# Optimization experiments

Measured on AMD Instinct MI355X. Metric: run time of the kernel, lower is better.

Reference implementation:

```python
import jax, jax.numpy as jnp
import numpy as np

D_MODEL = 1024
N_HEAD = 16
HEAD_DIM = D_MODEL // N_HEAD
ROPE_BASE = 10000.0


def _weight_quant(w):
    # BitNet b1.58 ternary weight quant with per-tensor absmean scale (STE).
    scale = jnp.clip(jnp.mean(jnp.abs(w)), 1e-5, None)
    wq = jnp.clip(jnp.round(w / scale), -1.0, 1.0) * scale
    return w + jax.lax.stop_gradient(wq - w)


def _act_quant(x):
    # Per-token int8 absmax activation quant (STE).
    scale = 127.0 / jnp.clip(jnp.max(jnp.abs(x), axis=-1, keepdims=True), 1e-5, None)
    xq = jnp.clip(jnp.round(x * scale), -128.0, 127.0) / scale
    return x + jax.lax.stop_gradient(xq - x)


def _bitlinear(x, w):
    # y = act_quant(x) @ weight_quant(w).T   (torch Linear convention, no bias)
    return _act_quant(x) @ _weight_quant(w).T


def _rope(x, pos):
    # x: [B, H, T, D]; half-split rotation.
    d = x.shape[-1]
    inv_freq = 1.0 / (ROPE_BASE ** (jnp.arange(0, d, 2, dtype=jnp.float32) / d))
    ang = pos[:, None].astype(jnp.float32) * inv_freq[None, :]  # [T, D/2]
    cos, sin = jnp.cos(ang), jnp.sin(ang)
    x1, x2 = x[..., : d // 2], x[..., d // 2 :]
    return jnp.concatenate([x1 * cos - x2 * sin, x1 * sin + x2 * cos], axis=-1)


def setup_inputs() -> dict:
    key = jax.random.key(0)
    k0, k1, k2, k3, k4 = jax.random.split(key, 5)
    B, T = 2, 2048
    s = 1.0 / np.sqrt(D_MODEL)
    return {
        "x": jax.random.normal(k0, (B, T, D_MODEL), dtype=jnp.float32),
        "Wq": jax.random.normal(k1, (D_MODEL, D_MODEL), dtype=jnp.float32) * s,
        "Wk": jax.random.normal(k2, (D_MODEL, D_MODEL), dtype=jnp.float32) * s,
        "Wv": jax.random.normal(k3, (D_MODEL, D_MODEL), dtype=jnp.float32) * s,
        "Wo": jax.random.normal(k4, (D_MODEL, D_MODEL), dtype=jnp.float32) * s,
    }


def reference(x, Wq, Wk, Wv, Wo):
    B, T, C = x.shape
    pos = jnp.arange(T)
    def heads(y):
        return y.reshape(B, T, N_HEAD, HEAD_DIM).transpose(0, 2, 1, 3)  # [B,H,T,D]
    q = _rope(heads(_bitlinear(x, Wq)), pos)
    k = _rope(heads(_bitlinear(x, Wk)), pos)
    v = heads(_bitlinear(x, Wv))
    scores = jnp.einsum("bhqd,bhkd->bhqk", q, k) / jnp.sqrt(jnp.float32(HEAD_DIM))
    causal = jnp.tril(jnp.ones((T, T), dtype=bool))
    scores = jnp.where(causal[None, None], scores, jnp.finfo(scores.dtype).min)
    att = jax.nn.softmax(scores, axis=-1)
    y = jnp.einsum("bhqk,bhkd->bhqd", att, v)  # [B,H,T,D]
    y = y.transpose(0, 2, 1, 3).reshape(B, T, C)
    return _bitlinear(y, Wo)
```

## Files before the change

kernel.cpp:

```cpp
#include <hip/hip_runtime.h>
#include <hip/hip_bf16.h>
#include <math.h>

typedef __bf16 bf16_t;
typedef signed char i8_t;
typedef __attribute__((ext_vector_type(8))) __bf16 bf16x8;
typedef __attribute__((ext_vector_type(4))) __bf16 bf16x4;
typedef __attribute__((ext_vector_type(4))) float f32x4;
typedef __attribute__((ext_vector_type(4))) int i32x4;

typedef __attribute__((address_space(3))) void lds_void_t;
typedef const __attribute__((address_space(1))) void glb_void_t;
#define GLOAD_LDS(g, l) __builtin_amdgcn_global_load_lds((glb_void_t*)(g), (lds_void_t*)(l), 16, 0, 0)

#define MFMA16(a,b,c) __builtin_amdgcn_mfma_f32_16x16x32_bf16(a,b,c,0,0,0)
#define MFMAI8(a,b,c) __builtin_amdgcn_mfma_i32_16x16x64_i8(a,b,c,0,0,0)

#if __has_builtin(__builtin_amdgcn_exp2f)
#define EXP2F(x) __builtin_amdgcn_exp2f(x)
#else
#define EXP2F(x) exp2f(x)
#endif

static constexpr int TSEQ = 2048;
static constexpr int CDIM = 1024;
#define NEG_BIG (-1.0e30f)
#define Q_PRESCALE 0.18033688011112042f
#define ROPE_C 0.41524101190971284f

__global__ __launch_bounds__(256) void wreduce(const float* __restrict__ W0, const float* __restrict__ W1,
                                               const float* __restrict__ W2, const float* __restrict__ W3,
                                               double* __restrict__ partial) {
  int w = blockIdx.x >> 6, b = blockIdx.x & 63;
  const float* W = (w==0)?W0:(w==1)?W1:(w==2)?W2:W3;
  const float* base = W + (size_t)b * 16384;
  double s = 0.0;
  for (int i = threadIdx.x * 4; i < 16384; i += 1024) {
    float4 v = *(const float4*)(base + i);
    s += (double)fabsf(v.x) + (double)fabsf(v.y) + (double)fabsf(v.z) + (double)fabsf(v.w);
  }
  #pragma unroll
  for (int off = 1; off < 64; off <<= 1) s += __shfl_xor(s, off);
  __shared__ double red[4];
  if ((threadIdx.x & 63) == 0) red[threadIdx.x >> 6] = s;
  __syncthreads();
  if (threadIdx.x == 0) partial[blockIdx.x] = red[0] + red[1] + red[2] + red[3];
}

__global__ __launch_bounds__(256) void prep(const float* __restrict__ W0, const float* __restrict__ W1,
                                            const float* __restrict__ W2, const float* __restrict__ W3,
                                            const double* __restrict__ partial, float* __restrict__ wscale,
                                            i8_t* __restrict__ wq_all,
                                            const float* __restrict__ xg, i8_t* __restrict__ xqg,
                                            float* __restrict__ rowfac, float2* __restrict__ ropetab) {
  int bid = blockIdx.x;
  if (bid < 4096) {
    int w = bid >> 10;
    double ssum = 0.0;
    for (int i = 0; i < 64; ++i) ssum += partial[w * 64 + i];
    float s = fmaxf((float)(ssum * (1.0 / 1048576.0)), 1e-5f);
    if ((bid & 1023) == 0 && threadIdx.x == 0) wscale[w] = s;
    const float* W = (w==0)?W0:(w==1)?W1:(w==2)?W2:W3;
    int off = ((bid & 1023) * 256 + threadIdx.x) * 4;
    float4 v = *(const float4*)(W + off);
    char4 q;
    q.x = (i8_t)(int)fminf(fmaxf(rintf(v.x / s), -1.f), 1.f);
    q.y = (i8_t)(int)fminf(fmaxf(rintf(v.y / s), -1.f), 1.f);
    q.z = (i8_t)(int)fminf(fmaxf(rintf(v.z / s), -1.f), 1.f);
    q.w = (i8_t)(int)fminf(fmaxf(rintf(v.w / s), -1.f), 1.f);
    *(char4*)(wq_all + (size_t)w * 1048576 + off) = q;
  } else if (bid < 8192) {
    int r = bid - 4096;
    float4 v = *(const float4*)(xg + (size_t)r * 1024 + threadIdx.x * 4);
    float mx = fmaxf(fmaxf(fabsf(v.x), fabsf(v.y)), fmaxf(fabsf(v.z), fabsf(v.w)));
    #pragma unroll
    for (int off = 1; off < 64; off <<= 1) mx = fmaxf(mx, __shfl_xor(mx, off));
    __shared__ float red[4];
    if ((threadIdx.x & 63) == 0) red[threadIdx.x >> 6] = mx;
    __syncthreads();
    mx = fmaxf(fmaxf(red[0], red[1]), fmaxf(red[2], red[3]));
    mx = fmaxf(mx, 1e-5f);
    float scale = 127.0f / mx;
    if (threadIdx.x == 0) rowfac[r] = mx * (1.0f / 127.0f);
    char4 q;
    q.x = (i8_t)(int)fminf(fmaxf(rintf(v.x * scale), -128.f), 127.f);
    q.y = (i8_t)(int)fminf(fmaxf(rintf(v.y * scale), -128.f), 127.f);
    q.z = (i8_t)(int)fminf(fmaxf(rintf(v.z * scale), -128.f), 127.f);
    q.w = (i8_t)(int)fminf(fmaxf(rintf(v.w * scale), -128.f), 127.f);
    *(char4*)(xqg + (size_t)r * 1024 + threadIdx.x * 4) = q;
  } else {
    int t = (bid - 8192) * 8 + (threadIdx.x >> 5);
    int ii = threadIdx.x & 31;
    float ang = (float)t * exp2f(-(float)ii * ROPE_C);
    float sn, cs;
    sincosf(ang, &sn, &cs);
    ropetab[t * 32 + ii] = make_float2(cs, sn);
  }
}

__global__ __launch_bounds__(256) void actquant(const float* __restrict__ xg, i8_t* __restrict__ xqg,
                                                float* __restrict__ rowfac) {
  int r = blockIdx.x;
  float4 v = *(const float4*)(xg + (size_t)r * 1024 + threadIdx.x * 4);
  float mx = fmaxf(fmaxf(fabsf(v.x), fabsf(v.y)), fmaxf(fabsf(v.z), fabsf(v.w)));
  #pragma unroll
  for (int off = 1; off < 64; off <<= 1) mx = fmaxf(mx, __shfl_xor(mx, off));
  __shared__ float red[4];
  if ((threadIdx.x & 63) == 0) red[threadIdx.x >> 6] = mx;
  __syncthreads();
  mx = fmaxf(fmaxf(red[0], red[1]), fmaxf(red[2], red[3]));
  mx = fmaxf(mx, 1e-5f);
  float scale = 127.0f / mx;
  if (threadIdx.x == 0) rowfac[r] = mx * (1.0f / 127.0f);
  char4 q;
  q.x = (i8_t)(int)fminf(fmaxf(rintf(v.x * scale), -128.f), 127.f);
  q.y = (i8_t)(int)fminf(fmaxf(rintf(v.y * scale), -128.f), 127.f);
  q.z = (i8_t)(int)fminf(fmaxf(rintf(v.z * scale), -128.f), 127.f);
  q.w = (i8_t)(int)fminf(fmaxf(rintf(v.w * scale), -128.f), 127.f);
  *(char4*)(xqg + (size_t)r * 1024 + threadIdx.x * 4) = q;
}

__global__ __launch_bounds__(256) void gemm_qkv(const i8_t* __restrict__ xq, const i8_t* __restrict__ wq_all,
                                                const float* __restrict__ wscale, const float* __restrict__ rowfac,
                                                const float2* __restrict__ ropetab,
                                                bf16_t* __restrict__ qb, bf16_t* __restrict__ kb,
                                                bf16_t* __restrict__ vtb) {
  const int z = blockIdx.z;
  const i8_t* Bw = wq_all + (size_t)z * 1048576;
  const int m0 = blockIdx.x * 128, n0 = blockIdx.y * 128;
  const int tid = threadIdx.x;
  const int wave = tid >> 6, lane = tid & 63, quad = lane >> 4, l16 = lane & 15;
  const int wm = wave >> 1, wn = wave & 1;
  __shared__ __align__(16) i8_t As[2][128 * 64];
  __shared__ __align__(16) i8_t Bs[2][128 * 64];
  i32x4 zero = {0, 0, 0, 0};
  i32x4 acc[4][4];
  #pragma unroll
  for (int i = 0; i < 4; ++i)
    #pragma unroll
    for (int j = 0; j < 4; ++j) acc[i][j] = zero;

  const int row_s = tid >> 2;
  const int cg16 = (((tid & 3) - (row_s >> 1)) & 3) * 16;
  const int sw16 = ((quad + (l16 >> 1)) & 3) * 16;

  #pragma unroll
  for (int v2 = 0; v2 < 2; ++v2) {
    int v = tid + v2 * 256;
    int row = row_s + v2 * 64;
    GLOAD_LDS(&xq[(size_t)(m0 + row) * 1024 + cg16], &As[0][v * 16]);
    GLOAD_LDS(&Bw[(size_t)(n0 + row) * 1024 + cg16], &Bs[0][v * 16]);
  }
  __syncthreads();

  #pragma unroll 2
  for (int kt = 0; kt < 16; ++kt) {
    const int cur = kt & 1;
    if (kt < 15) {
      #pragma unroll
      for (int v2 = 0; v2 < 2; ++v2) {
        int v = tid + v2 * 256;
        int row = row_s + v2 * 64;
        GLOAD_LDS(&xq[(size_t)(m0 + row) * 1024 + (kt + 1) * 64 + cg16], &As[cur ^ 1][v * 16]);
        GLOAD_LDS(&Bw[(size_t)(n0 + row) * 1024 + (kt + 1) * 64 + cg16], &Bs[cur ^ 1][v * 16]);
      }
    }
    i32x4 af[4], bfr[4];
    #pragma unroll
    for (int i = 0; i < 4; ++i) af[i] = *(const i32x4*)&As[cur][(wm * 64 + i * 16 + l16) * 64 + sw16];
    #pragma unroll
    for (int j = 0; j < 4; ++j) bfr[j] = *(const i32x4*)&Bs[cur][(wn * 64 + j * 16 + l16) * 64 + sw16];
    if (z == 2) {
      #pragma unroll
      for (int i = 0; i < 4; ++i)
        #pragma unroll
        for (int j = 0; j < 4; ++j) acc[i][j] = MFMAI8(bfr[i], af[j], acc[i][j]);
    } else {
      #pragma unroll
      for (int i = 0; i < 4; ++i)
        #pragma unroll
        for (int j = 0; j < 4; ++j) acc[i][j] = MFMAI8(af[i], bfr[j], acc[i][j]);
    }
    __syncthreads();
  }
  float ws = wscale[z] * (z == 0 ? Q_PRESCALE : 1.0f);
  if (z <= 1) {
    bf16_t* dst = (z == 0) ? qb : kb;
    const int h = (n0 >> 6) + wn;
    #pragma unroll
    for (int i = 0; i < 4; ++i) {
      #pragma unroll
      for (int r = 0; r < 4; ++r) {
        int m = m0 + wm * 64 + i * 16 + quad * 4 + r;
        float rf = rowfac[m] * ws;
        int b = m >> 11, t = m & 2047;
        bf16_t* drow = dst + (((size_t)b * 16 + h) * 2048 + t) * 64;
        #pragma unroll
        for (int j = 0; j < 2; ++j) {
          int dd1 = j * 16 + l16;
          float2 cs2 = ropetab[t * 32 + dd1];
          float v1 = (float)acc[i][j][r] * rf;
          float v2 = (float)acc[i][j + 2][r] * rf;
          drow[dd1]      = (bf16_t)(v1 * cs2.x - v2 * cs2.y);
          drow[dd1 + 32] = (bf16_t)(v1 * cs2.y + v2 * cs2.x);
        }
      }
    }
  } else {
    const int b = m0 >> 11;
    const int tbase = (m0 & 2047) + wm * 64;
    float rfj[4];
    #pragma unroll
    for (int j = 0; j < 4; ++j) rfj[j] = rowfac[m0 + wm * 64 + j * 16 + l16] * ws;
    #pragma unroll
    for (int i = 0; i < 4; ++i) {
      #pragma unroll
      for (int r = 0; r < 4; ++r) {
        int nrow = n0 + wn * 64 + i * 16 + quad * 4 + r;
        int h = nrow >> 6, dd = nrow & 63;
        bf16_t* vrow = vtb + (((size_t)b * 16 + h) * 64 + dd) * 2048 + tbase;
        #pragma unroll
        for (int j = 0; j < 4; ++j) vrow[j * 16 + l16] = (bf16_t)((float)acc[i][j][r] * rfj[j]);
      }
    }
  }
}

__global__ __launch_bounds__(256) void gemm_out(const i8_t* __restrict__ yq, const i8_t* __restrict__ wo,
                                                const float* __restrict__ wscale, const float* __restrict__ rowfac,
                                                float* __restrict__ out) {
  const int m0 = blockIdx.x * 128, n0 = blockIdx.y * 128;
  const int tid = threadIdx.x;
  const int wave = tid >> 6, lane = tid & 63, quad = lane >> 4, l16 = lane & 15;
  const int wm = wave >> 1, wn = wave & 1;
  __shared__ __align__(16) i8_t As[2][128 * 64];
  __shared__ __align__(16) i8_t Bs[2][128 * 64];
  i32x4 zero = {0, 0, 0, 0};
  i32x4 acc[4][4];
  #pragma unroll
  for (int i = 0; i < 4; ++i)
    #pragma unroll
    for (int j = 0; j < 4; ++j) acc[i][j] = zero;

  const int row_s = tid >> 2;
  const int cg16 = (((tid & 3) - (row_s >> 1)) & 3) * 16;
  const int sw16 = ((quad + (l16 >> 1)) & 3) * 16;

  #pragma unroll
  for (int v2 = 0; v2 < 2; ++v2) {
    int v = tid + v2 * 256;
    int row = row_s + v2 * 64;
    GLOAD_LDS(&yq[(size_t)(m0 + row) * 1024 + cg16], &As[0][v * 16]);
    GLOAD_LDS(&wo[(size_t)(n0 + row) * 1024 + cg16], &Bs[0][v * 16]);
  }
  __syncthreads();

  #pragma unroll 2
  for (int kt = 0; kt < 16; ++kt) {
    const int cur = kt & 1;
    if (kt < 15) {
      #pragma unroll
      for (int v2 = 0; v2 < 2; ++v2) {
        int v = tid + v2 * 256;
        int row = row_s + v2 * 64;
        GLOAD_LDS(&yq[(size_t)(m0 + row) * 1024 + (kt + 1) * 64 + cg16], &As[cur ^ 1][v * 16]);
        GLOAD_LDS(&wo[(size_t)(n0 + row) * 1024 + (kt + 1) * 64 + cg16], &Bs[cur ^ 1][v * 16]);
      }
    }
    i32x4 af[4], bfr[4];
    #pragma unroll
    for (int i = 0; i < 4; ++i) af[i] = *(const i32x4*)&As[cur][(wm * 64 + i * 16 + l16) * 64 + sw16];
    #pragma unroll
    for (int j = 0; j < 4; ++j) bfr[j] = *(const i32x4*)&Bs[cur][(wn * 64 + j * 16 + l16) * 64 + sw16];
    #pragma unroll
    for (int i = 0; i < 4; ++i)
      #pragma unroll
      for (int j = 0; j < 4; ++j) acc[i][j] = MFMAI8(af[i], bfr[j], acc[i][j]);
    __syncthreads();
  }
  float ws = wscale[3];
  #pragma unroll
  for (int i = 0; i < 4; ++i) {
    #pragma unroll
    for (int r = 0; r < 4; ++r) {
      int m = m0 + wm * 64 + i * 16 + quad * 4 + r;
      float rf = rowfac[m] * ws;
      #pragma unroll
      for (int j = 0; j < 4; ++j) {
        int n = n0 + wn * 64 + j * 16 + l16;
        out[(size_t)m * 1024 + n] = (float)acc[i][j][r] * rf;
      }
    }
  }
}

__global__ __launch_bounds__(512) void flash_attn(const bf16_t* __restrict__ qg, const bf16_t* __restrict__ kg,
                                                  const bf16_t* __restrict__ vtg, float* __restrict__ yf) {
  const int lid = (int)blockIdx.y * 8 + (int)blockIdx.x;
  const int p  = (lid >> 3) & 7;
  const int bh = (lid & 7) * 4 + (lid >> 6);
  const int tid = threadIdx.x;
  const int wave = tid >> 6, lane = tid & 63;
  const int quad = lane >> 4, l16 = lane & 15;

  __shared__ __align__(16) bf16_t Kb[2][64 * 64];
  __shared__ __align__(16) bf16_t Vb[2][64 * 64];
  __shared__ __align__(16) bf16_t Pl[8][16 * 72];

  const int b = bh >> 4, h = bh & 15;
  bf16_t* Pw = &Pl[wave][0];

  const int r0 = tid >> 3, cblk = tid & 7;
  const int ldsOff0 = r0 * 64 + ((cblk ^ (r0 & 7)) * 8);
  const size_t bhbase = (size_t)bh * 131072;
  const bf16_t* kbase0 = kg + bhbase + r0 * 64 + cblk * 8;
  const bf16_t* vbase0 = vtg + bhbase + r0 * 2048 + cblk * 8;

  int kf_off[4][2];
  #pragma unroll
  for (int n = 0; n < 4; ++n)
    #pragma unroll
    for (int c = 0; c < 2; ++c)
      kf_off[n][c] = (n * 16 + l16) * 64 + (((c * 4 + quad) ^ (l16 & 7)) * 8);

  bf16x8 ones;
  #pragma unroll
  for (int j = 0; j < 8; ++j) ones[j] = (bf16_t)1.0f;
  f32x4 zero = {0.f, 0.f, 0.f, 0.f};

  bf16x8 kpre = *(const bf16x8*)(kbase0);
  bf16x8 vpre = *(const bf16x8*)(vbase0);

  int cum = 0;
  #pragma unroll 1
  for (int tsel = 0; tsel < 2; ++tsel) {
    const int qt = tsel ? (15 - p) : p;
    const int kcmax = 2 * qt + 1;
    const int qbw = qt * 128 + wave * 16;

    const bf16_t* qrowp = qg + ((size_t)bh * TSEQ + qbw + l16) * 64;
    bf16x8 aq0 = *(const bf16x8*)(qrowp + quad * 8);
    bf16x8 aq1 = *(const bf16x8*)(qrowp + 32 + quad * 8);

    f32x4 o[4], o5;
    #pragma unroll
    for (int i = 0; i < 4; ++i) o[i] = zero;
    o5 = zero;

    #pragma unroll 1
    for (int kc = 0; kc <= kcmax; ++kc, ++cum) {
      const int buf = cum & 1;
      bf16_t* Kt = &Kb[buf][0];
      bf16_t* Vt = &Vb[buf][0];
      *(bf16x8*)&Kt[ldsOff0] = kpre;
      *(bf16x8*)&Vt[ldsOff0] = vpre;
      __syncthreads();
      int nkc = (kc < kcmax) ? (kc + 1) : ((tsel == 0) ? 0 : -1);
      if (nkc >= 0) {
        kpre = *(const bf16x8*)(kbase0 + nkc * 4096);
        vpre = *(const bf16x8*)(vbase0 + nkc * 64);
      }

      if (kc * 64 > qbw + 15) continue;

      f32x4 s[4];
      __builtin_amdgcn_s_setprio(1);
      #pragma unroll
      for (int n = 0; n < 4; ++n) {
        bf16x8 bk0 = *(const bf16x8*)&Kt[kf_off[n][0]];
        bf16x8 bk1 = *(const bf16x8*)&Kt[kf_off[n][1]];
        s[n] = MFMA16(aq1, bk1, MFMA16(aq0, bk0, zero));
      }
      __builtin_amdgcn_s_setprio(0);
      if (kc * 64 + 63 > qbw) {
        #pragma unroll
        for (int n = 0; n < 4; ++n)
          #pragma unroll
          for (int r = 0; r < 4; ++r) {
            int kpos = kc * 64 + n * 16 + l16;
            int qpos = qbw + quad * 4 + r;
            if (kpos > qpos) s[n][r] = NEG_BIG;
          }
      }
      #pragma unroll
      for (int n = 0; n < 4; ++n)
        #pragma unroll
        for (int r = 0; r < 4; ++r)
          Pw[(quad * 4 + r) * 72 + n * 16 + l16] = (bf16_t)EXP2F(s[n][r]);

      bf16x8 ap0 = *(const bf16x8*)&Pw[l16 * 72 + quad * 8];
      bf16x8 ap1 = *(const bf16x8*)&Pw[l16 * 72 + 32 + quad * 8];
      __builtin_amdgcn_s_setprio(1);
      #pragma unroll
      for (int nh = 0; nh < 4; ++nh) {
        bf16x8 bv0 = *(const bf16x8*)&Vt[kf_off[nh][0]];
        bf16x8 bv1 = *(const bf16x8*)&Vt[kf_off[nh][1]];
        o[nh] = MFMA16(ap1, bv1, MFMA16(ap0, bv0, o[nh]));
      }
      o5 = MFMA16(ap1, ones, MFMA16(ap0, ones, o5));
      __builtin_amdgcn_s_setprio(0);
    }

    #pragma unroll
    for (int r = 0; r < 4; ++r) {
      float invl = 1.0f / o5[r];
      int t = qbw + quad * 4 + r;
      float* yrow = yf + ((size_t)b * TSEQ + t) * CDIM + h * 64;
      #pragma unroll
      for (int nh = 0; nh < 4; ++nh) yrow[nh * 16 + l16] = o[nh][r] * invl;
    }
  }
}

extern "C" void kernel_launch(void* const* d_in, const int* in_sizes, int n_in,
                              void* d_out, int out_size, void* d_ws, size_t ws_size,
                              hipStream_t stream) {
  const float* x  = (const float*)d_in[0];
  const float* Wq = (const float*)d_in[1];
  const float* Wk = (const float*)d_in[2];
  const float* Wv = (const float*)d_in[3];
  const float* Wo = (const float*)d_in[4];
  float* out = (float*)d_out;

  char* ws = (char*)d_ws;
  double* wpartial = (double*)(ws);
  float* wscale   = (float*)(ws + 4096);
  float* rowfacx  = (float*)(ws + 8192);
  float* rowfacy  = (float*)(ws + 8192 + 16384);
  i8_t* wq_all    = (i8_t*)(ws + 65536);
  i8_t* xq        = wq_all + 4194304;
  bf16_t* qb      = (bf16_t*)(xq + 4194304);
  bf16_t* kb      = qb + 4194304;
  bf16_t* vtb     = kb + 4194304;
  float*  yf      = (float*)(vtb + 4194304);
  float2* ropetab = (float2*)(yf + 4194304);
  i8_t* yq        = xq;

  wreduce<<<256, 256, 0, stream>>>(Wq, Wk, Wv, Wo, wpartial);
  prep<<<8448, 256, 0, stream>>>(Wq, Wk, Wv, Wo, wpartial, wscale, wq_all, x, xq, rowfacx, ropetab);
  gemm_qkv<<<dim3(32, 8, 3), 256, 0, stream>>>(xq, wq_all, wscale, rowfacx, ropetab, qb, kb, vtb);
  flash_attn<<<dim3(8, 32), 512, 0, stream>>>(qb, kb, vtb, yf);
  actquant<<<4096, 256, 0, stream>>>(yf, yq, rowfacy);
  gemm_out<<<dim3(32, 8), 256, 0, stream>>>(yq, wq_all + 3 * 1048576, wscale, rowfacy, out);
}
```

Measured before the change: 175.9 us.

## Enlarge flash attention KV tile from 64 to 128 keys per iteration

The attention loop now stages 128 keys of K and V per iteration instead of 64. This halves the number of barrier-synchronized iterations and removes the per-wave skip of fully masked tiles, since 128-key tiles line up with 128-row query tiles. Only the final tile needs the causal mask. In exchange LDS use roughly doubles, the prefetch registers double, and waves near the start of a query tile compute some masked work they previously skipped.

```diff
diff --git a/kernel.cpp b/kernel.cpp
--- a/kernel.cpp
+++ b/kernel.cpp
@@ -303,39 +303,38 @@
   const int wave = tid >> 6, lane = tid & 63;
   const int quad = lane >> 4, l16 = lane & 15;
 
-  __shared__ __align__(16) bf16_t Kb[2][64 * 64];
-  __shared__ __align__(16) bf16_t Vb[2][64 * 64];
-  __shared__ __align__(16) bf16_t Pl[8][16 * 72];
+  __shared__ __align__(16) bf16_t Kb[2][128 * 64];
+  __shared__ __align__(16) bf16_t Vb[2][64 * 128];
+  __shared__ __align__(16) bf16_t Pl[8][16 * 136];
 
   const int b = bh >> 4, h = bh & 15;
   bf16_t* Pw = &Pl[wave][0];
 
-  const int r0 = tid >> 3, cblk = tid & 7;
-  const int ldsOff0 = r0 * 64 + ((cblk ^ (r0 & 7)) * 8);
+  const int r0k = tid >> 3, cblk = tid & 7;
+  const int ldsKA = r0k * 64 + ((cblk ^ (r0k & 7)) * 8);
+  const int rv = tid >> 4, cv = tid & 15;
+  const int ldsVA = rv * 128 + ((cv ^ (rv & 7)) * 8);
+
   const size_t bhbase = (size_t)bh * 131072;
-  const bf16_t* kbase0 = kg + bhbase + r0 * 64 + cblk * 8;
-  const bf16_t* vbase0 = vtg + bhbase + r0 * 2048 + cblk * 8;
-
-  int kf_off[4][2];
-  #pragma unroll
-  for (int n = 0; n < 4; ++n)
-    #pragma unroll
-    for (int c = 0; c < 2; ++c)
-      kf_off[n][c] = (n * 16 + l16) * 64 + (((c * 4 + quad) ^ (l16 & 7)) * 8);
-
+  const bf16_t* kbaseA = kg + bhbase + r0k * 64 + cblk * 8;
+  const bf16_t* vbaseA = vtg + bhbase + rv * 2048 + cv * 8;
+
+  const int xk = (l16 & 7);
   bf16x8 ones;
   #pragma unroll
   for (int j = 0; j < 8; ++j) ones[j] = (bf16_t)1.0f;
   f32x4 zero = {0.f, 0.f, 0.f, 0.f};
 
-  bf16x8 kpre = *(const bf16x8*)(kbase0);
-  bf16x8 vpre = *(const bf16x8*)(vbase0);
+  bf16x8 kpreA = *(const bf16x8*)(kbaseA);
+  bf16x8 kpreB = *(const bf16x8*)(kbaseA + 4096);
+  bf16x8 vpreA = *(const bf16x8*)(vbaseA);
+  bf16x8 vpreB = *(const bf16x8*)(vbaseA + 65536);
 
   int cum = 0;
   #pragma unroll 1
   for (int tsel = 0; tsel < 2; ++tsel) {
     const int qt = tsel ? (15 - p) : p;
-    const int kcmax = 2 * qt + 1;
+    const int kcmax = qt;
     const int qbw = qt * 128 + wave * 16;
 
     const bf16_t* qrowp = qg + ((size_t)bh * TSEQ + qbw + l16) * 64;
@@ -352,52 +351,58 @@
       const int buf = cum & 1;
       bf16_t* Kt = &Kb[buf][0];
       bf16_t* Vt = &Vb[buf][0];
-      *(bf16x8*)&Kt[ldsOff0] = kpre;
-      *(bf16x8*)&Vt[ldsOff0] = vpre;
+      *(bf16x8*)&Kt[ldsKA]        = kpreA;
+      *(bf16x8*)&Kt[ldsKA + 4096] = kpreB;
+      *(bf16x8*)&Vt[ldsVA]        = vpreA;
+      *(bf16x8*)&Vt[ldsVA + 4096] = vpreB;
       __syncthreads();
       int nkc = (kc < kcmax) ? (kc + 1) : ((tsel == 0) ? 0 : -1);
       if (nkc >= 0) {
-        kpre = *(const bf16x8*)(kbase0 + nkc * 4096);
-        vpre = *(const bf16x8*)(vbase0 + nkc * 64);
-      }
-
-      if (kc * 64 > qbw + 15) continue;
-
-      f32x4 s[4];
+        kpreA = *(const bf16x8*)(kbaseA + nkc * 8192);
+        kpreB = *(const bf16x8*)(kbaseA + nkc * 8192 + 4096);
+        vpreA = *(const bf16x8*)(vbaseA + nkc * 128);
+        vpreB = *(const bf16x8*)(vbaseA + nkc * 128 + 65536);
+      }
+
+      f32x4 s[8];
       __builtin_amdgcn_s_setprio(1);
       #pragma unroll
-      for (int n = 0; n < 4; ++n) {
-        bf16x8 bk0 = *(const bf16x8*)&Kt[kf_off[n][0]];
-        bf16x8 bk1 = *(const bf16x8*)&Kt[kf_off[n][1]];
+      for (int n = 0; n < 8; ++n) {
+        bf16x8 bk0 = *(const bf16x8*)&Kt[l16 * 64 + ((quad       ^ xk) * 8) + n * 1024];
+        bf16x8 bk1 = *(const bf16x8*)&Kt[l16 * 64 + (((4 + quad) ^ xk) * 8) + n * 1024];
         s[n] = MFMA16(aq1, bk1, MFMA16(aq0, bk0, zero));
       }
       __builtin_amdgcn_s_setprio(0);
-      if (kc * 64 + 63 > qbw) {
-        #pragma unroll
-        for (int n = 0; n < 4; ++n)
+
+      if (kc == kcmax) {
+        #pragma unroll
+        for (int n = 0; n < 8; ++n)
           #pragma unroll
           for (int r = 0; r < 4; ++r) {
-            int kpos = kc * 64 + n * 16 + l16;
+            int kpos = kc * 128 + n * 16 + l16;
             int qpos = qbw + quad * 4 + r;
             if (kpos > qpos) s[n][r] = NEG_BIG;
           }
       }
       #pragma unroll
-      for (int n = 0; n < 4; ++n)
+      for (int n = 0; n < 8; ++n)
         #pragma unroll
         for (int r = 0; r < 4; ++r)
-          Pw[(quad * 4 + r) * 72 + n * 16 + l16] = (bf16_t)EXP2F(s[n][r]);
-
-      bf16x8 ap0 = *(const bf16x8*)&Pw[l16 * 72 + quad * 8];
-      bf16x8 ap1 = *(const bf16x8*)&Pw[l16 * 72 + 32 + quad * 8];
+          Pw[(quad * 4 + r) * 136 + n * 16 + l16] = (bf16_t)EXP2F(s[n][r]);
+
+      bf16x8 ap[4];
+      #pragma unroll
+      for (int c = 0; c < 4; ++c) ap[c] = *(const bf16x8*)&Pw[l16 * 136 + c * 32 + quad * 8];
       __builtin_amdgcn_s_setprio(1);
       #pragma unroll
-      for (int nh = 0; nh < 4; ++nh) {
-        bf16x8 bv0 = *(const bf16x8*)&Vt[kf_off[nh][0]];
-        bf16x8 bv1 = *(const bf16x8*)&Vt[kf_off[nh][1]];
-        o[nh] = MFMA16(ap1, bv1, MFMA16(ap0, bv0, o[nh]));
-      }
-      o5 = MFMA16(ap1, ones, MFMA16(ap0, ones, o5));
+      for (int c = 0; c < 4; ++c) {
+        #pragma unroll
+        for (int nh = 0; nh < 4; ++nh) {
+          bf16x8 bv = *(const bf16x8*)&Vt[l16 * 128 + (((c * 4 + quad) ^ xk) * 8) + nh * 2048];
+          o[nh] = MFMA16(ap[c], bv, o[nh]);
+        }
+        o5 = MFMA16(ap[c], ones, o5);
+      }
       __builtin_amdgcn_s_setprio(0);
     }
 
```

Measured after the change: 174.7 us. No clear change (-0.7%).

## Split attention KV range across two blocks and combine partials in actquant

Applied to the files above, without the earlier changes.

Flash attention now launches twice as many blocks, each handling alternate KV chunks (even or odd) for the same query tiles. Each block writes unnormalized partial outputs and denominators, which actquant sums and normalizes before quantizing. This raises parallelism from 256 to 512 blocks to fill more CUs, at the cost of extra global writes and reads of a second fp32 partial buffer. It relies on there being no running-max subtraction (fixed-scale exp2), so the partials can be added directly.

```diff
diff --git a/kernel.cpp b/kernel.cpp
--- a/kernel.cpp
+++ b/kernel.cpp
@@ -98,10 +98,22 @@
   }
 }
 
-__global__ __launch_bounds__(256) void actquant(const float* __restrict__ xg, i8_t* __restrict__ xqg,
-                                                float* __restrict__ rowfac) {
+__global__ __launch_bounds__(256) void actquant(const float* __restrict__ yf0, const float* __restrict__ yf1,
+                                                const float* __restrict__ den0, const float* __restrict__ den1,
+                                                i8_t* __restrict__ xqg, float* __restrict__ rowfac) {
   int r = blockIdx.x;
-  float4 v = *(const float4*)(xg + (size_t)r * 1024 + threadIdx.x * 4);
+  int b = r >> 11, t = r & 2047;
+  int h = threadIdx.x >> 4;
+  size_t idx = (size_t)r * 1024 + threadIdx.x * 4;
+  float4 v0 = *(const float4*)(yf0 + idx);
+  float4 v1 = *(const float4*)(yf1 + idx);
+  size_t di = (size_t)(b * 16 + h) * 2048 + t;
+  float inv = 1.0f / (den0[di] + den1[di]);
+  float4 v;
+  v.x = (v0.x + v1.x) * inv;
+  v.y = (v0.y + v1.y) * inv;
+  v.z = (v0.z + v1.z) * inv;
+  v.w = (v0.w + v1.w) * inv;
   float mx = fmaxf(fmaxf(fabsf(v.x), fabsf(v.y)), fmaxf(fabsf(v.z), fabsf(v.w)));
   #pragma unroll
   for (int off = 1; off < 64; off <<= 1) mx = fmaxf(mx, __shfl_xor(mx, off));
@@ -295,10 +307,15 @@
 }
 
 __global__ __launch_bounds__(512) void flash_attn(const bf16_t* __restrict__ qg, const bf16_t* __restrict__ kg,
-                                                  const bf16_t* __restrict__ vtg, float* __restrict__ yf) {
+                                                  const bf16_t* __restrict__ vtg,
+                                                  float* __restrict__ yf0, float* __restrict__ yf1,
+                                                  float* __restrict__ den0, float* __restrict__ den1) {
   const int lid = (int)blockIdx.y * 8 + (int)blockIdx.x;
-  const int p  = (lid >> 3) & 7;
-  const int bh = (lid & 7) * 4 + (lid >> 6);
+  const int par = (lid >> 3) & 1;
+  const int p   = (lid >> 4) & 7;
+  const int bh  = (lid & 7) * 4 + (lid >> 7);
+  float* __restrict__ yo = par ? yf1 : yf0;
+  float* __restrict__ dn = par ? den1 : den0;
   const int tid = threadIdx.x;
   const int wave = tid >> 6, lane = tid & 63;
   const int quad = lane >> 4, l16 = lane & 15;
@@ -328,8 +345,8 @@
   for (int j = 0; j < 8; ++j) ones[j] = (bf16_t)1.0f;
   f32x4 zero = {0.f, 0.f, 0.f, 0.f};
 
-  bf16x8 kpre = *(const bf16x8*)(kbase0);
-  bf16x8 vpre = *(const bf16x8*)(vbase0);
+  bf16x8 kpre = *(const bf16x8*)(kbase0 + par * 4096);
+  bf16x8 vpre = *(const bf16x8*)(vbase0 + par * 64);
 
   int cum = 0;
   #pragma unroll 1
@@ -348,14 +365,14 @@
     o5 = zero;
 
     #pragma unroll 1
-    for (int kc = 0; kc <= kcmax; ++kc, ++cum) {
+    for (int kc = par; kc <= kcmax; kc += 2, ++cum) {
       const int buf = cum & 1;
       bf16_t* Kt = &Kb[buf][0];
       bf16_t* Vt = &Vb[buf][0];
       *(bf16x8*)&Kt[ldsOff0] = kpre;
       *(bf16x8*)&Vt[ldsOff0] = vpre;
       __syncthreads();
-      int nkc = (kc < kcmax) ? (kc + 1) : ((tsel == 0) ? 0 : -1);
+      int nkc = (kc + 2 <= kcmax) ? (kc + 2) : ((tsel == 0) ? par : -1);
       if (nkc >= 0) {
         kpre = *(const bf16x8*)(kbase0 + nkc * 4096);
         vpre = *(const bf16x8*)(vbase0 + nkc * 64);
@@ -403,11 +420,11 @@
 
     #pragma unroll
     for (int r = 0; r < 4; ++r) {
-      float invl = 1.0f / o5[r];
       int t = qbw + quad * 4 + r;
-      float* yrow = yf + ((size_t)b * TSEQ + t) * CDIM + h * 64;
-      #pragma unroll
-      for (int nh = 0; nh < 4; ++nh) yrow[nh * 16 + l16] = o[nh][r] * invl;
+      float* yrow = yo + ((size_t)b * TSEQ + t) * CDIM + h * 64;
+      #pragma unroll
+      for (int nh = 0; nh < 4; ++nh) yrow[nh * 16 + l16] = o[nh][r];
+      if (l16 == 0) dn[(size_t)bh * TSEQ + t] = o5[r];
     }
   }
 }
@@ -432,14 +449,17 @@
   bf16_t* qb      = (bf16_t*)(xq + 4194304);
   bf16_t* kb      = qb + 4194304;
   bf16_t* vtb     = kb + 4194304;
-  float*  yf      = (float*)(vtb + 4194304);
-  float2* ropetab = (float2*)(yf + 4194304);
+  float*  yf0     = (float*)(vtb + 4194304);
+  float2* ropetab = (float2*)(yf0 + 4194304);
+  float*  yf1     = (float*)((char*)ropetab + 524288);
+  float*  den0    = (float*)((char*)yf1 + 16777216);
+  float*  den1    = den0 + 65536;
   i8_t* yq        = xq;
 
   wreduce<<<256, 256, 0, stream>>>(Wq, Wk, Wv, Wo, wpartial);
   prep<<<8448, 256, 0, stream>>>(Wq, Wk, Wv, Wo, wpartial, wscale, wq_all, x, xq, rowfacx, ropetab);
   gemm_qkv<<<dim3(32, 8, 3), 256, 0, stream>>>(xq, wq_all, wscale, rowfacx, ropetab, qb, kb, vtb);
-  flash_attn<<<dim3(8, 32), 512, 0, stream>>>(qb, kb, vtb, yf);
-  actquant<<<4096, 256, 0, stream>>>(yf, yq, rowfacy);
+  flash_attn<<<dim3(8, 64), 512, 0, stream>>>(qb, kb, vtb, yf0, yf1, den0, den1);
+  actquant<<<4096, 256, 0, stream>>>(yf0, yf1, den0, den1, yq, rowfacy);
   gemm_out<<<dim3(32, 8), 256, 0, stream>>>(yq, wq_all + 3 * 1048576, wscale, rowfacy, out);
 }
```

New measurement: 172.4 us, median of 2. 1.02x faster.

## Load K/V MFMA fragments directly from global memory instead of LDS staging

Applied to the files above, without the earlier changes.

Drops the double-buffered shared-memory staging of K and V tiles and the per-iteration block barrier in flash attention. Each wave now reads its MFMA B-operand fragments straight from global memory (relying on L1/L2 caching), and each wave can stop its key loop early with break instead of idling at barriers. This removes LDS writes, swizzle bookkeeping and __syncthreads, but costs 8x redundant global/cache traffic across waves and more exposed load latency because there is no software prefetch.

```diff
diff --git a/kernel.cpp b/kernel.cpp
--- a/kernel.cpp
+++ b/kernel.cpp
@@ -303,35 +303,20 @@
   const int wave = tid >> 6, lane = tid & 63;
   const int quad = lane >> 4, l16 = lane & 15;
 
-  __shared__ __align__(16) bf16_t Kb[2][64 * 64];
-  __shared__ __align__(16) bf16_t Vb[2][64 * 64];
   __shared__ __align__(16) bf16_t Pl[8][16 * 72];
 
   const int b = bh >> 4, h = bh & 15;
   bf16_t* Pw = &Pl[wave][0];
 
-  const int r0 = tid >> 3, cblk = tid & 7;
-  const int ldsOff0 = r0 * 64 + ((cblk ^ (r0 & 7)) * 8);
   const size_t bhbase = (size_t)bh * 131072;
-  const bf16_t* kbase0 = kg + bhbase + r0 * 64 + cblk * 8;
-  const bf16_t* vbase0 = vtg + bhbase + r0 * 2048 + cblk * 8;
-
-  int kf_off[4][2];
-  #pragma unroll
-  for (int n = 0; n < 4; ++n)
-    #pragma unroll
-    for (int c = 0; c < 2; ++c)
-      kf_off[n][c] = (n * 16 + l16) * 64 + (((c * 4 + quad) ^ (l16 & 7)) * 8);
+  const bf16_t* kfb = kg + bhbase + l16 * 64 + quad * 8;
+  const bf16_t* vfb = vtg + bhbase + (size_t)l16 * 2048 + quad * 8;
 
   bf16x8 ones;
   #pragma unroll
   for (int j = 0; j < 8; ++j) ones[j] = (bf16_t)1.0f;
   f32x4 zero = {0.f, 0.f, 0.f, 0.f};
 
-  bf16x8 kpre = *(const bf16x8*)(kbase0);
-  bf16x8 vpre = *(const bf16x8*)(vbase0);
-
-  int cum = 0;
   #pragma unroll 1
   for (int tsel = 0; tsel < 2; ++tsel) {
     const int qt = tsel ? (15 - p) : p;
@@ -348,27 +333,18 @@
     o5 = zero;
 
     #pragma unroll 1
-    for (int kc = 0; kc <= kcmax; ++kc, ++cum) {
-      const int buf = cum & 1;
-      bf16_t* Kt = &Kb[buf][0];
-      bf16_t* Vt = &Vb[buf][0];
-      *(bf16x8*)&Kt[ldsOff0] = kpre;
-      *(bf16x8*)&Vt[ldsOff0] = vpre;
-      __syncthreads();
-      int nkc = (kc < kcmax) ? (kc + 1) : ((tsel == 0) ? 0 : -1);
-      if (nkc >= 0) {
-        kpre = *(const bf16x8*)(kbase0 + nkc * 4096);
-        vpre = *(const bf16x8*)(vbase0 + nkc * 64);
-      }
-
-      if (kc * 64 > qbw + 15) continue;
+    for (int kc = 0; kc <= kcmax; ++kc) {
+      if (kc * 64 > qbw + 15) break;
+
+      const bf16_t* kck = kfb + kc * 4096;
+      const bf16_t* vck = vfb + kc * 64;
 
       f32x4 s[4];
       __builtin_amdgcn_s_setprio(1);
       #pragma unroll
       for (int n = 0; n < 4; ++n) {
-        bf16x8 bk0 = *(const bf16x8*)&Kt[kf_off[n][0]];
-        bf16x8 bk1 = *(const bf16x8*)&Kt[kf_off[n][1]];
+        bf16x8 bk0 = *(const bf16x8*)(kck + n * 1024);
+        bf16x8 bk1 = *(const bf16x8*)(kck + n * 1024 + 32);
         s[n] = MFMA16(aq1, bk1, MFMA16(aq0, bk0, zero));
       }
       __builtin_amdgcn_s_setprio(0);
@@ -393,8 +369,8 @@
       __builtin_amdgcn_s_setprio(1);
       #pragma unroll
       for (int nh = 0; nh < 4; ++nh) {
-        bf16x8 bv0 = *(const bf16x8*)&Vt[kf_off[nh][0]];
-        bf16x8 bv1 = *(const bf16x8*)&Vt[kf_off[nh][1]];
+        bf16x8 bv0 = *(const bf16x8*)(vck + nh * 32768);
+        bf16x8 bv1 = *(const bf16x8*)(vck + nh * 32768 + 32);
         o[nh] = MFMA16(ap1, bv1, MFMA16(ap0, bv0, o[nh]));
       }
       o5 = MFMA16(ap1, ones, MFMA16(ap0, ones, o5));
```

Measured after the change: 256.5 us. 1.46x slower.
